# Optimization experiments

Hardware: AMD Instinct MI355X
Metric: run time of the kernel (lower is better)

## Reference

```python
import jax, jax.numpy as jnp
import numpy as np

COS_EPS = 1e-08


def setup_inputs() -> dict:
    key = jax.random.key(0)
    k1, k2, k3, k4, k5 = jax.random.split(key, 5)
    B, N, C = 4, 4096, 128
    q_node = jax.random.normal(k1, (B, N, C), dtype=jnp.float32)
    k_node = jax.random.normal(k2, (B, N, C), dtype=jnp.float32)
    v_node = jax.random.normal(k3, (B, N, C), dtype=jnp.float32)
    # shared Linear(h_dim, h_dim): torch default init scale ~ 1/sqrt(C)
    W = jax.random.normal(k4, (C, C), dtype=jnp.float32) / jnp.sqrt(jnp.float32(C))
    b = jax.random.normal(k5, (C,), dtype=jnp.float32) / jnp.sqrt(jnp.float32(C))
    return {"q_node": q_node, "k_node": k_node, "v_node": v_node, "W": W, "b": b}


def reference(q_node, k_node, v_node, W, b):
    # shared projection applied to q, k, v
    q = jnp.einsum('bnc,cd->bnd', q_node, W.T) + b
    k = jnp.einsum('bnc,cd->bnd', k_node, W.T) + b
    v = jnp.einsum('bnc,cd->bnd', v_node, W.T) + b
    # cosine similarity scores: [B, Nq, Nk]
    qn = jnp.linalg.norm(q, axis=2, keepdims=True)        # [B, Nq, 1]
    kn = jnp.linalg.norm(k, axis=2, keepdims=True)        # [B, Nk, 1]
    scores = jnp.einsum('bqc,bkc->bqk', q, k)
    cos_sim = scores / (qn * jnp.swapaxes(kn, 1, 2) + COS_EPS)
    # sum-normalization (not softmax)
    edge_weight = cos_sim / (cos_sim.sum(axis=2, keepdims=True) + 1e-08)
    # weighted aggregation: [B, Nq, C]
    return jnp.einsum('bqk,bkc->bqc', edge_weight, v)
```

## Files before the change

kernel.cpp:

```cpp
#include <hip/hip_runtime.h>

#define BB 4
#define NN 4096
#define CC 128
#define NROWS (BB * NN)

#define QN_OFF  0
#define QP_OFF  (QN_OFF + NROWS)
#define MM_OFF  (QP_OFF + NROWS * CC)
#define KS_OFF  (MM_OFF + BB * CC * CC)
#define PP_OFF  (KS_OFF + BB * CC)
#define KP_OFF  (PP_OFF + 256 * CC * CC)

__device__ __forceinline__ void fma4(float4& a, const float4 x,
    const float4 w0, const float4 w1, const float4 w2, const float4 w3)
{
    a.x += x.x * w0.x + x.y * w1.x + x.z * w2.x + x.w * w3.x;
    a.y += x.x * w0.y + x.y * w1.y + x.z * w2.y + x.w * w3.y;
    a.z += x.x * w0.z + x.y * w1.z + x.z * w2.z + x.w * w3.z;
    a.w += x.x * w0.w + x.y * w1.w + x.z * w2.w + x.w * w3.w;
}

__device__ __forceinline__ float dot4(const float4 x, const float4 k)
{
    return x.x * k.x + x.y * k.y + x.z * k.z + x.w * k.w;
}

__global__ __launch_bounds__(512, 2) void projpb_kernel(
    const float* __restrict__ q_node, const float* __restrict__ k_node,
    const float* __restrict__ v_node, const float* __restrict__ W,
    const float* __restrict__ bias, float* __restrict__ ws)
{
    __shared__ float S[CC * CC];
    __shared__ float4 red[512];
    const int tid = threadIdx.x;

    for (int e = tid; e < CC * CC; e += 512) {
        int d = e >> 7, c = e & 127;
        S[(c << 7) + ((((d >> 2) ^ (c & 31)) << 2) | (d & 3))] = W[e];
    }

    const int blk  = blockIdx.x;
    const int base = blk * 64;
    const int dg = tid & 31;
    const int rg = tid >> 5;

    float4 bias4 = ((const float4*)bias)[dg];
    float4 acc[8];
#pragma unroll
    for (int i = 0; i < 8; i++) acc[i] = bias4;

    __syncthreads();

    const float4* Qv = (const float4*)(q_node + (size_t)(base + rg * 4) * CC);
    const float4* Kv = (const float4*)(k_node + (size_t)(base + rg * 4) * CC);
    const float4* Sv = (const float4*)S;

#define LW(s0, s1, s2, s3, c)                              \
    s0 = Sv[(((c) + 0) << 5) + (dg ^ (((c) + 0) & 31))];   \
    s1 = Sv[(((c) + 1) << 5) + (dg ^ (((c) + 1) & 31))];   \
    s2 = Sv[(((c) + 2) << 5) + (dg ^ (((c) + 2) & 31))];   \
    s3 = Sv[(((c) + 3) << 5) + (dg ^ (((c) + 3) & 31))];
#define LX(xq, xk, c)                                      \
    { const int c4_ = (c) >> 2;                            \
      xq[0] = Qv[c4_];      xq[1] = Qv[32 + c4_];          \
      xq[2] = Qv[64 + c4_]; xq[3] = Qv[96 + c4_];          \
      xk[0] = Kv[c4_];      xk[1] = Kv[32 + c4_];          \
      xk[2] = Kv[64 + c4_]; xk[3] = Kv[96 + c4_]; }
#define FM(w0, w1, w2, w3, xq, xk)                         \
    fma4(acc[0], xq[0], w0, w1, w2, w3);                   \
    fma4(acc[1], xq[1], w0, w1, w2, w3);                   \
    fma4(acc[2], xq[2], w0, w1, w2, w3);                   \
    fma4(acc[3], xq[3], w0, w1, w2, w3);                   \
    fma4(acc[4], xk[0], w0, w1, w2, w3);                   \
    fma4(acc[5], xk[1], w0, w1, w2, w3);                   \
    fma4(acc[6], xk[2], w0, w1, w2, w3);                   \
    fma4(acc[7], xk[3], w0, w1, w2, w3);

    {
        float4 wA0, wA1, wA2, wA3, wB0, wB1, wB2, wB3;
        float4 xqA[4], xkA[4], xqB[4], xkB[4];

        LW(wA0, wA1, wA2, wA3, 0)
        LX(xqA, xkA, 0)
        for (int c = 0; c <= CC - 16; c += 8) {
            LW(wB0, wB1, wB2, wB3, c + 4)
            LX(xqB, xkB, c + 4)
            FM(wA0, wA1, wA2, wA3, xqA, xkA)
            LW(wA0, wA1, wA2, wA3, c + 8)
            LX(xqA, xkA, c + 8)
            FM(wB0, wB1, wB2, wB3, xqB, xkB)
        }
        LW(wB0, wB1, wB2, wB3, CC - 4)
        LX(xqB, xkB, CC - 4)
        FM(wA0, wA1, wA2, wA3, xqA, xkA)
        FM(wB0, wB1, wB2, wB3, xqB, xkB)
    }
#undef LW
#undef LX
#undef FM

#pragma unroll
    for (int i = 0; i < 4; i++) {
        const int rq = base + rg * 4 + i;
        float ss = acc[i].x * acc[i].x + acc[i].y * acc[i].y
                 + acc[i].z * acc[i].z + acc[i].w * acc[i].w;
#pragma unroll
        for (int off = 16; off > 0; off >>= 1) ss += __shfl_xor(ss, off, 32);
        ((float4*)(ws + QP_OFF + (size_t)rq * CC))[dg] = acc[i];
        if (dg == 0) ws[QN_OFF + rq] = sqrtf(ss);
    }

    __syncthreads();

    float* Khs = S;
    float* Vs  = S + 8192;

#pragma unroll
    for (int i = 0; i < 4; i++) {
        float ss = acc[4 + i].x * acc[4 + i].x + acc[4 + i].y * acc[4 + i].y
                 + acc[4 + i].z * acc[4 + i].z + acc[4 + i].w * acc[4 + i].w;
#pragma unroll
        for (int off = 16; off > 0; off >>= 1) ss += __shfl_xor(ss, off, 32);
        float inv = 1.0f / sqrtf(ss);
        float4 o = acc[4 + i];
        o.x *= inv; o.y *= inv; o.z *= inv; o.w *= inv;
        ((float4*)(Khs + (rg * 4 + i) * CC))[dg] = o;
    }

    const int c4v = tid & 31, nrv = tid >> 5;
    const float* Vp = v_node + (size_t)base * CC;
#pragma unroll
    for (int i = 0; i < 4; i++) {
        int n = nrv + i * 16;
        ((float4*)(Vs + n * CC))[c4v] = ((const float4*)(Vp + (size_t)n * CC))[c4v];
    }
    __syncthreads();

    float4 ksum4 = make_float4(0.f, 0.f, 0.f, 0.f);
#pragma unroll
    for (int i = 0; i < 4; i++) {
        int n = nrv + i * 16;
        float4 kv = ((const float4*)(Khs + n * CC))[c4v];
        ksum4.x += kv.x; ksum4.y += kv.y; ksum4.z += kv.z; ksum4.w += kv.w;
    }

    const int dg2 = tid & 15, cg = tid >> 4;
    float a2[4][8];
#pragma unroll
    for (int i = 0; i < 4; i++)
#pragma unroll
        for (int j = 0; j < 8; j++) a2[i][j] = 0.f;

#define P2L(ka, va, vb, n)                                  \
    ka = *(const float4*)(Khs + (n) * CC + 4 * cg);         \
    va = *(const float4*)(Vs + (n) * CC + 4 * dg2);         \
    vb = *(const float4*)(Vs + (n) * CC + 64 + 4 * dg2);
#define P2F(ka, va, vb)                                     \
    {  float kc[4] = {ka.x, ka.y, ka.z, ka.w};              \
       float vd[8] = {va.x, va.y, va.z, va.w,               \
                      vb.x, vb.y, vb.z, vb.w};              \
       _Pragma("unroll")                                    \
       for (int i = 0; i < 4; i++)                          \
           { _Pragma("unroll")                              \
             for (int j = 0; j < 8; j++)                    \
                 a2[i][j] += kc[i] * vd[j]; } }

    {
        float4 kaA, vaA, vbA, kaB, vaB, vbB;
        P2L(kaA, vaA, vbA, 0)
        for (int n = 0; n <= 60; n += 2) {
            P2L(kaB, vaB, vbB, n + 1)
            P2F(kaA, vaA, vbA)
            P2L(kaA, vaA, vbA, n + 2)
            P2F(kaB, vaB, vbB)
        }
        P2L(kaB, vaB, vbB, 63)
        P2F(kaA, vaA, vbA)
        P2F(kaB, vaB, vbB)
    }
#undef P2L
#undef P2F

    float* pp = ws + PP_OFF + (size_t)blk * (CC * CC);
#pragma unroll
    for (int i = 0; i < 4; i++) {
        int c = 4 * cg + i;
        *(float4*)(pp + c * CC + 4 * dg2) =
            make_float4(a2[i][0], a2[i][1], a2[i][2], a2[i][3]);
        *(float4*)(pp + c * CC + 64 + 4 * dg2) =
            make_float4(a2[i][4], a2[i][5], a2[i][6], a2[i][7]);
    }

    red[nrv * 32 + c4v] = ksum4;
    __syncthreads();
    if (tid < 32) {
        float4 sm = red[tid];
#pragma unroll
        for (int i = 1; i < 16; i++) {
            float4 t = red[i * 32 + tid];
            sm.x += t.x; sm.y += t.y; sm.z += t.z; sm.w += t.w;
        }
        ((float4*)(ws + KP_OFF + (size_t)blk * CC))[tid] = sm;
    }
}

__global__ __launch_bounds__(256) void mchain_kernel(const float* __restrict__ W,
                                                     const float* __restrict__ bias,
                                                     float* __restrict__ ws)
{
    __shared__ float4 W4s[CC * 32];
    __shared__ float m0row[2][CC];
    __shared__ float kpart[4];
    __shared__ float ksl[2];
    const int tid = threadIdx.x;
    const int b = blockIdx.y, x = blockIdx.x;
    const int c0 = x * 2;

    for (int idx = tid; idx < CC * 32; idx += 256) {
        int e = idx >> 5, d4 = idx & 31;
        W4s[(e << 5) + (d4 ^ (e & 31))] = ((const float4*)W)[idx];
    }

    {
        const int r = tid >> 7, d = tid & 127;
        const float* pp = ws + PP_OFF + (size_t)(b * 64) * (CC * CC)
                        + (size_t)(c0 + r) * CC + d;
        float a0 = 0.f, a1 = 0.f, a2 = 0.f, a3 = 0.f;
#pragma unroll 8
        for (int p = 0; p < 64; p += 4) {
            a0 += pp[(size_t)(p + 0) * (CC * CC)];
            a1 += pp[(size_t)(p + 1) * (CC * CC)];
            a2 += pp[(size_t)(p + 2) * (CC * CC)];
            a3 += pp[(size_t)(p + 3) * (CC * CC)];
        }
        m0row[r][d] = (a0 + a1) + (a2 + a3);
    }

    {
        const int rr = tid >> 7, p = tid & 127;
        float v = 0.f;
        if (p < 64) v = ws[KP_OFF + (size_t)(b * 64 + p) * CC + c0 + rr];
#pragma unroll
        for (int off = 32; off > 0; off >>= 1) v += __shfl_xor(v, off, 64);
        if ((tid & 63) == 0) kpart[tid >> 6] = v;
    }
    __syncthreads();
    if (tid < 2) {
        float s = kpart[tid * 2] + kpart[tid * 2 + 1];
        ksl[tid] = s;
        ws[KS_OFF + b * CC + c0 + tid] = s;
    }
    __syncthreads();

    const int r = tid >> 7, e = tid & 127;
    const float4* mr = (const float4*)m0row[r];
    float m = 0.f;
#pragma unroll
    for (int d4 = 0; d4 < 32; d4++) {
        float4 a4 = mr[d4];
        float4 w4 = W4s[(e << 5) + (d4 ^ (e & 31))];
        m += a4.x * w4.x + a4.y * w4.y + a4.z * w4.z + a4.w * w4.w;
    }
    m += ksl[r] * bias[e];
    ws[MM_OFF + (size_t)b * CC * CC + (size_t)(c0 + r) * CC + e] = m;
}

__global__ __launch_bounds__(512, 2) void out_kernel(const float* __restrict__ ws,
                                                     float* __restrict__ out)
{
    __shared__ float Ml[CC * CC];

    const int blk = blockIdx.x;
    const int b = blk >> 6;
    const int r0 = (blk & 63) * 64;
    const float* M = ws + MM_OFF + (size_t)b * CC * CC;
    const int tid = threadIdx.x;

    for (int e = tid; e < CC * CC / 4; e += 512)
        ((float4*)Ml)[e] = ((const float4*)M)[e];

    const float4* Ks4 = (const float4*)(ws + KS_OFF + b * CC);
    const int dg = tid & 31, rg = tid >> 5;
    const int row = r0 + rg * 4;
    const float4* Qv = (const float4*)(ws + QP_OFF + ((size_t)b * NN + row) * CC);
    const float4* Mv = (const float4*)Ml;

    float4 acc[4];
    float s[4];
#pragma unroll
    for (int i = 0; i < 4; i++) {
        acc[i] = make_float4(0.f, 0.f, 0.f, 0.f);
        s[i] = 0.f;
    }

    __syncthreads();

#define OLW(m0, m1, m2, m3, ks, c)               \
    m0 = Mv[(((c) + 0) << 5) + dg];              \
    m1 = Mv[(((c) + 1) << 5) + dg];              \
    m2 = Mv[(((c) + 2) << 5) + dg];              \
    m3 = Mv[(((c) + 3) << 5) + dg];              \
    ks = Ks4[(c) >> 2];
#define OLX(xv, c)                                 \
    { const int c4_ = (c) >> 2;                    \
      xv[0] = Qv[c4_];      xv[1] = Qv[32 + c4_];  \
      xv[2] = Qv[64 + c4_]; xv[3] = Qv[96 + c4_]; }
#define OFM(m0, m1, m2, m3, ks, xv)                  \
    _Pragma("unroll")                                \
    for (int i_ = 0; i_ < 4; i_++) {                 \
        fma4(acc[i_], xv[i_], m0, m1, m2, m3);       \
        s[i_] += dot4(xv[i_], ks);                   \
    }

    {
        float4 mA0, mA1, mA2, mA3, mB0, mB1, mB2, mB3;
        float4 ksA, ksB, xA[4], xB[4];
        OLW(mA0, mA1, mA2, mA3, ksA, 0)
        OLX(xA, 0)
        for (int c = 0; c <= CC - 16; c += 8) {
            OLW(mB0, mB1, mB2, mB3, ksB, c + 4)
            OLX(xB, c + 4)
            OFM(mA0, mA1, mA2, mA3, ksA, xA)
            OLW(mA0, mA1, mA2, mA3, ksA, c + 8)
            OLX(xA, c + 8)
            OFM(mB0, mB1, mB2, mB3, ksB, xB)
        }
        OLW(mB0, mB1, mB2, mB3, ksB, CC - 4)
        OLX(xB, CC - 4)
        OFM(mA0, mA1, mA2, mA3, ksA, xA)
        OFM(mB0, mB1, mB2, mB3, ksB, xB)
    }
#undef OLW
#undef OLX
#undef OFM

    float* op = out + ((size_t)b * NN + row) * CC;
    const float* qn = ws + QN_OFF + (size_t)b * NN + row;
#pragma unroll
    for (int i = 0; i < 4; i++) {
        float inv = 1.0f / (s[i] + 1e-8f * qn[i]);
        float4 o = acc[i];
        o.x *= inv; o.y *= inv; o.z *= inv; o.w *= inv;
        ((float4*)(op + (size_t)i * CC))[dg] = o;
    }
}

extern "C" void kernel_launch(void* const* d_in, const int* in_sizes, int n_in,
                              void* d_out, int out_size, void* d_ws, size_t ws_size,
                              hipStream_t stream)
{
    const float* q_node = (const float*)d_in[0];
    const float* k_node = (const float*)d_in[1];
    const float* v_node = (const float*)d_in[2];
    const float* W      = (const float*)d_in[3];
    const float* bias   = (const float*)d_in[4];
    float* out = (float*)d_out;
    float* ws  = (float*)d_ws;

    projpb_kernel<<<256, 512, 0, stream>>>(q_node, k_node, v_node, W, bias, ws);
    mchain_kernel<<<dim3(64, BB), 256, 0, stream>>>(W, bias, ws);
    out_kernel<<<256, 512, 0, stream>>>(ws, out);
}
```

Measured before the change: 130.6 us.

## Fuse three kernels into one persistent kernel with software grid barriers

Merges the projection/partial-product, M-chain, and output kernels into a single 256-block launch separated by atomic-counter grid barriers, with a memset resetting the counters each call. The M-chain stage is remapped onto 512-thread blocks by splitting the 64-way partial sum into two halves. The aim is to remove two kernel launch gaps and their tail effects. In exchange it relies on all 256 blocks being co-resident, which holds on a 256-CU part, and adds a memset plus spin-wait cost.

```diff
diff --git a/kernel.cpp b/kernel.cpp
--- a/kernel.cpp
+++ b/kernel.cpp
@@ -11,6 +11,9 @@
 #define KS_OFF  (MM_OFF + BB * CC * CC)
 #define PP_OFF  (KS_OFF + BB * CC)
 #define KP_OFF  (PP_OFF + 256 * CC * CC)
+#define BAR_OFF (KP_OFF + 256 * CC)
+
+#define NBLK 256
 
 __device__ __forceinline__ void fma4(float4& a, const float4 x,
     const float4 w0, const float4 w1, const float4 w2, const float4 w3)
@@ -26,35 +29,51 @@
     return x.x * k.x + x.y * k.y + x.z * k.z + x.w * k.w;
 }
 
-__global__ __launch_bounds__(512, 2) void projpb_kernel(
+__device__ __forceinline__ void grid_barrier(unsigned* ctr)
+{
+    __syncthreads();
+    __threadfence();
+    if (threadIdx.x == 0) {
+        atomicAdd(ctr, 1u);
+        while (atomicAdd(ctr, 0u) < NBLK) {}
+    }
+    __syncthreads();
+    __threadfence();
+}
+
+__global__ __launch_bounds__(512, 2) void fused_kernel(
     const float* __restrict__ q_node, const float* __restrict__ k_node,
     const float* __restrict__ v_node, const float* __restrict__ W,
-    const float* __restrict__ bias, float* __restrict__ ws)
+    const float* __restrict__ bias, float* __restrict__ ws,
+    float* __restrict__ out)
 {
     __shared__ float S[CC * CC];
     __shared__ float4 red[512];
+    unsigned* bar = (unsigned*)(ws + BAR_OFF);
+
     const int tid = threadIdx.x;
-
-    for (int e = tid; e < CC * CC; e += 512) {
-        int d = e >> 7, c = e & 127;
-        S[(c << 7) + ((((d >> 2) ^ (c & 31)) << 2) | (d & 3))] = W[e];
-    }
-
-    const int blk  = blockIdx.x;
-    const int base = blk * 64;
-    const int dg = tid & 31;
-    const int rg = tid >> 5;
-
-    float4 bias4 = ((const float4*)bias)[dg];
-    float4 acc[8];
-#pragma unroll
-    for (int i = 0; i < 8; i++) acc[i] = bias4;
-
-    __syncthreads();
-
-    const float4* Qv = (const float4*)(q_node + (size_t)(base + rg * 4) * CC);
-    const float4* Kv = (const float4*)(k_node + (size_t)(base + rg * 4) * CC);
-    const float4* Sv = (const float4*)S;
+    const int blk = blockIdx.x;
+
+    {
+        for (int e = tid; e < CC * CC; e += 512) {
+            int d = e >> 7, c = e & 127;
+            S[(c << 7) + ((((d >> 2) ^ (c & 31)) << 2) | (d & 3))] = W[e];
+        }
+
+        const int base = blk * 64;
+        const int dg = tid & 31;
+        const int rg = tid >> 5;
+
+        float4 bias4 = ((const float4*)bias)[dg];
+        float4 acc[8];
+#pragma unroll
+        for (int i = 0; i < 8; i++) acc[i] = bias4;
+
+        __syncthreads();
+
+        const float4* Qv = (const float4*)(q_node + (size_t)(base + rg * 4) * CC);
+        const float4* Kv = (const float4*)(k_node + (size_t)(base + rg * 4) * CC);
+        const float4* Sv = (const float4*)S;
 
 #define LW(s0, s1, s2, s3, c)                              \
     s0 = Sv[(((c) + 0) << 5) + (dg ^ (((c) + 0) & 31))];   \
@@ -77,83 +96,83 @@
     fma4(acc[6], xk[2], w0, w1, w2, w3);                   \
     fma4(acc[7], xk[3], w0, w1, w2, w3);
 
-    {
-        float4 wA0, wA1, wA2, wA3, wB0, wB1, wB2, wB3;
-        float4 xqA[4], xkA[4], xqB[4], xkB[4];
-
-        LW(wA0, wA1, wA2, wA3, 0)
-        LX(xqA, xkA, 0)
-        for (int c = 0; c <= CC - 16; c += 8) {
-            LW(wB0, wB1, wB2, wB3, c + 4)
-            LX(xqB, xkB, c + 4)
+        {
+            float4 wA0, wA1, wA2, wA3, wB0, wB1, wB2, wB3;
+            float4 xqA[4], xkA[4], xqB[4], xkB[4];
+
+            LW(wA0, wA1, wA2, wA3, 0)
+            LX(xqA, xkA, 0)
+            for (int c = 0; c <= CC - 16; c += 8) {
+                LW(wB0, wB1, wB2, wB3, c + 4)
+                LX(xqB, xkB, c + 4)
+                FM(wA0, wA1, wA2, wA3, xqA, xkA)
+                LW(wA0, wA1, wA2, wA3, c + 8)
+                LX(xqA, xkA, c + 8)
+                FM(wB0, wB1, wB2, wB3, xqB, xkB)
+            }
+            LW(wB0, wB1, wB2, wB3, CC - 4)
+            LX(xqB, xkB, CC - 4)
             FM(wA0, wA1, wA2, wA3, xqA, xkA)
-            LW(wA0, wA1, wA2, wA3, c + 8)
-            LX(xqA, xkA, c + 8)
             FM(wB0, wB1, wB2, wB3, xqB, xkB)
         }
-        LW(wB0, wB1, wB2, wB3, CC - 4)
-        LX(xqB, xkB, CC - 4)
-        FM(wA0, wA1, wA2, wA3, xqA, xkA)
-        FM(wB0, wB1, wB2, wB3, xqB, xkB)
-    }
 #undef LW
 #undef LX
 #undef FM
 
 #pragma unroll
-    for (int i = 0; i < 4; i++) {
-        const int rq = base + rg * 4 + i;
-        float ss = acc[i].x * acc[i].x + acc[i].y * acc[i].y
-                 + acc[i].z * acc[i].z + acc[i].w * acc[i].w;
-#pragma unroll
-        for (int off = 16; off > 0; off >>= 1) ss += __shfl_xor(ss, off, 32);
-        ((float4*)(ws + QP_OFF + (size_t)rq * CC))[dg] = acc[i];
-        if (dg == 0) ws[QN_OFF + rq] = sqrtf(ss);
-    }
-
-    __syncthreads();
-
-    float* Khs = S;
-    float* Vs  = S + 8192;
-
-#pragma unroll
-    for (int i = 0; i < 4; i++) {
-        float ss = acc[4 + i].x * acc[4 + i].x + acc[4 + i].y * acc[4 + i].y
-                 + acc[4 + i].z * acc[4 + i].z + acc[4 + i].w * acc[4 + i].w;
-#pragma unroll
-        for (int off = 16; off > 0; off >>= 1) ss += __shfl_xor(ss, off, 32);
-        float inv = 1.0f / sqrtf(ss);
-        float4 o = acc[4 + i];
-        o.x *= inv; o.y *= inv; o.z *= inv; o.w *= inv;
-        ((float4*)(Khs + (rg * 4 + i) * CC))[dg] = o;
-    }
-
-    const int c4v = tid & 31, nrv = tid >> 5;
-    const float* Vp = v_node + (size_t)base * CC;
-#pragma unroll
-    for (int i = 0; i < 4; i++) {
-        int n = nrv + i * 16;
-        ((float4*)(Vs + n * CC))[c4v] = ((const float4*)(Vp + (size_t)n * CC))[c4v];
-    }
-    __syncthreads();
-
-    float4 ksum4 = make_float4(0.f, 0.f, 0.f, 0.f);
-#pragma unroll
-    for (int i = 0; i < 4; i++) {
-        int n = nrv + i * 16;
-        float4 kv = ((const float4*)(Khs + n * CC))[c4v];
-        ksum4.x += kv.x; ksum4.y += kv.y; ksum4.z += kv.z; ksum4.w += kv.w;
-    }
-
-    const int dg2 = tid & 15, cg = tid >> 4;
-    float a2[4][8];
-#pragma unroll
-    for (int i = 0; i < 4; i++)
-#pragma unroll
-        for (int j = 0; j < 8; j++) a2[i][j] = 0.f;
+        for (int i = 0; i < 4; i++) {
+            const int rq = base + rg * 4 + i;
+            float ss = acc[i].x * acc[i].x + acc[i].y * acc[i].y
+                     + acc[i].z * acc[i].z + acc[i].w * acc[i].w;
+#pragma unroll
+            for (int off = 16; off > 0; off >>= 1) ss += __shfl_xor(ss, off, 32);
+            ((float4*)(ws + QP_OFF + (size_t)rq * CC))[dg] = acc[i];
+            if (dg == 0) ws[QN_OFF + rq] = sqrtf(ss);
+        }
+
+        __syncthreads();
+
+        float* Khs = S;
+        float* Vs  = S + 8192;
+
+#pragma unroll
+        for (int i = 0; i < 4; i++) {
+            float ss = acc[4 + i].x * acc[4 + i].x + acc[4 + i].y * acc[4 + i].y
+                     + acc[4 + i].z * acc[4 + i].z + acc[4 + i].w * acc[4 + i].w;
+#pragma unroll
+            for (int off = 16; off > 0; off >>= 1) ss += __shfl_xor(ss, off, 32);
+            float inv = 1.0f / sqrtf(ss);
+            float4 o = acc[4 + i];
+            o.x *= inv; o.y *= inv; o.z *= inv; o.w *= inv;
+            ((float4*)(Khs + (rg * 4 + i) * CC))[dg] = o;
+        }
+
+        const int c4v = tid & 31, nrv = tid >> 5;
+        const float* Vp = v_node + (size_t)base * CC;
+#pragma unroll
+        for (int i = 0; i < 4; i++) {
+            int n = nrv + i * 16;
+            ((float4*)(Vs + n * CC))[c4v] = ((const float4*)(Vp + (size_t)n * CC))[c4v];
+        }
+        __syncthreads();
+
+        float4 ksum4 = make_float4(0.f, 0.f, 0.f, 0.f);
+#pragma unroll
+        for (int i = 0; i < 4; i++) {
+            int n = nrv + i * 16;
+            float4 kv = ((const float4*)(Khs + n * CC))[c4v];
+            ksum4.x += kv.x; ksum4.y += kv.y; ksum4.z += kv.z; ksum4.w += kv.w;
+        }
+
+        const int dg2 = tid & 15, cg2 = tid >> 4;
+        float a2[4][8];
+#pragma unroll
+        for (int i = 0; i < 4; i++)
+#pragma unroll
+            for (int j = 0; j < 8; j++) a2[i][j] = 0.f;
 
 #define P2L(ka, va, vb, n)                                  \
-    ka = *(const float4*)(Khs + (n) * CC + 4 * cg);         \
+    ka = *(const float4*)(Khs + (n) * CC + 4 * cg2);        \
     va = *(const float4*)(Vs + (n) * CC + 4 * dg2);         \
     vb = *(const float4*)(Vs + (n) * CC + 64 + 4 * dg2);
 #define P2F(ka, va, vb)                                     \
@@ -166,135 +185,139 @@
              for (int j = 0; j < 8; j++)                    \
                  a2[i][j] += kc[i] * vd[j]; } }
 
-    {
-        float4 kaA, vaA, vbA, kaB, vaB, vbB;
-        P2L(kaA, vaA, vbA, 0)
-        for (int n = 0; n <= 60; n += 2) {
-            P2L(kaB, vaB, vbB, n + 1)
+        {
+            float4 kaA, vaA, vbA, kaB, vaB, vbB;
+            P2L(kaA, vaA, vbA, 0)
+            for (int n = 0; n <= 60; n += 2) {
+                P2L(kaB, vaB, vbB, n + 1)
+                P2F(kaA, vaA, vbA)
+                P2L(kaA, vaA, vbA, n + 2)
+                P2F(kaB, vaB, vbB)
+            }
+            P2L(kaB, vaB, vbB, 63)
             P2F(kaA, vaA, vbA)
-            P2L(kaA, vaA, vbA, n + 2)
             P2F(kaB, vaB, vbB)
         }
-        P2L(kaB, vaB, vbB, 63)
-        P2F(kaA, vaA, vbA)
-        P2F(kaB, vaB, vbB)
-    }
 #undef P2L
 #undef P2F
 
-    float* pp = ws + PP_OFF + (size_t)blk * (CC * CC);
-#pragma unroll
-    for (int i = 0; i < 4; i++) {
-        int c = 4 * cg + i;
-        *(float4*)(pp + c * CC + 4 * dg2) =
-            make_float4(a2[i][0], a2[i][1], a2[i][2], a2[i][3]);
-        *(float4*)(pp + c * CC + 64 + 4 * dg2) =
-            make_float4(a2[i][4], a2[i][5], a2[i][6], a2[i][7]);
-    }
-
-    red[nrv * 32 + c4v] = ksum4;
-    __syncthreads();
-    if (tid < 32) {
-        float4 sm = red[tid];
-#pragma unroll
-        for (int i = 1; i < 16; i++) {
-            float4 t = red[i * 32 + tid];
-            sm.x += t.x; sm.y += t.y; sm.z += t.z; sm.w += t.w;
-        }
-        ((float4*)(ws + KP_OFF + (size_t)blk * CC))[tid] = sm;
-    }
-}
-
-__global__ __launch_bounds__(256) void mchain_kernel(const float* __restrict__ W,
-                                                     const float* __restrict__ bias,
-                                                     float* __restrict__ ws)
-{
-    __shared__ float4 W4s[CC * 32];
-    __shared__ float m0row[2][CC];
-    __shared__ float kpart[4];
-    __shared__ float ksl[2];
-    const int tid = threadIdx.x;
-    const int b = blockIdx.y, x = blockIdx.x;
-    const int c0 = x * 2;
-
-    for (int idx = tid; idx < CC * 32; idx += 256) {
-        int e = idx >> 5, d4 = idx & 31;
-        W4s[(e << 5) + (d4 ^ (e & 31))] = ((const float4*)W)[idx];
-    }
+        float* pp = ws + PP_OFF + (size_t)blk * (CC * CC);
+#pragma unroll
+        for (int i = 0; i < 4; i++) {
+            int c = 4 * cg2 + i;
+            *(float4*)(pp + c * CC + 4 * dg2) =
+                make_float4(a2[i][0], a2[i][1], a2[i][2], a2[i][3]);
+            *(float4*)(pp + c * CC + 64 + 4 * dg2) =
+                make_float4(a2[i][4], a2[i][5], a2[i][6], a2[i][7]);
+        }
+
+        red[nrv * 32 + c4v] = ksum4;
+        __syncthreads();
+        if (tid < 32) {
+            float4 sm = red[tid];
+#pragma unroll
+            for (int i = 1; i < 16; i++) {
+                float4 t = red[i * 32 + tid];
+                sm.x += t.x; sm.y += t.y; sm.z += t.z; sm.w += t.w;
+            }
+            ((float4*)(ws + KP_OFF + (size_t)blk * CC))[tid] = sm;
+        }
+    }
+
+    grid_barrier(bar);
 
     {
-        const int r = tid >> 7, d = tid & 127;
-        const float* pp = ws + PP_OFF + (size_t)(b * 64) * (CC * CC)
-                        + (size_t)(c0 + r) * CC + d;
-        float a0 = 0.f, a1 = 0.f, a2 = 0.f, a3 = 0.f;
+        float4* W4s   = (float4*)S;
+        float*  m0p   = (float*)red;
+        float*  kpart = m0p + 512;
+        float*  ksl   = kpart + 2;
+        float*  m0row = ksl + 2;
+
+        const int x = blk & 63, b2 = blk >> 6;
+        const int c0 = x * 2;
+
+        for (int idx = tid; idx < CC * 32; idx += 512) {
+            int e = idx >> 5, d4 = idx & 31;
+            W4s[(e << 5) + (d4 ^ (e & 31))] = ((const float4*)W)[idx];
+        }
+
+        {
+            const int r2 = tid >> 7;
+            const int r = r2 & 1, h = r2 >> 1;
+            const int d = tid & 127;
+            const float* pp = ws + PP_OFF
+                            + (size_t)(b2 * 64 + h * 32) * (CC * CC)
+                            + (size_t)(c0 + r) * CC + d;
+            float a0 = 0.f, a1 = 0.f, a2 = 0.f, a3 = 0.f;
 #pragma unroll 8
-        for (int p = 0; p < 64; p += 4) {
-            a0 += pp[(size_t)(p + 0) * (CC * CC)];
-            a1 += pp[(size_t)(p + 1) * (CC * CC)];
-            a2 += pp[(size_t)(p + 2) * (CC * CC)];
-            a3 += pp[(size_t)(p + 3) * (CC * CC)];
-        }
-        m0row[r][d] = (a0 + a1) + (a2 + a3);
-    }
+            for (int p = 0; p < 32; p += 4) {
+                a0 += pp[(size_t)(p + 0) * (CC * CC)];
+                a1 += pp[(size_t)(p + 1) * (CC * CC)];
+                a2 += pp[(size_t)(p + 2) * (CC * CC)];
+                a3 += pp[(size_t)(p + 3) * (CC * CC)];
+            }
+            m0p[r2 * CC + d] = (a0 + a1) + (a2 + a3);
+        }
+
+        if (tid < 128) {
+            const int rr = tid >> 6, p = tid & 63;
+            float v = ws[KP_OFF + (size_t)(b2 * 64 + p) * CC + c0 + rr];
+#pragma unroll
+            for (int off = 32; off > 0; off >>= 1) v += __shfl_xor(v, off, 64);
+            if ((tid & 63) == 0) kpart[rr] = v;
+        }
+        __syncthreads();
+
+        if (tid < 256) {
+            const int r = tid >> 7, d = tid & 127;
+            m0row[r * CC + d] = m0p[r * CC + d] + m0p[(r + 2) * CC + d];
+        }
+        if (tid < 2) {
+            ksl[tid] = kpart[tid];
+            ws[KS_OFF + b2 * CC + c0 + tid] = kpart[tid];
+        }
+        __syncthreads();
+
+        if (tid < 256) {
+            const int r = tid >> 7, e = tid & 127;
+            const float4* mr = (const float4*)(m0row + r * CC);
+            float m = 0.f;
+#pragma unroll
+            for (int d4 = 0; d4 < 32; d4++) {
+                float4 a4 = mr[d4];
+                float4 w4 = W4s[(e << 5) + (d4 ^ (e & 31))];
+                m += a4.x * w4.x + a4.y * w4.y + a4.z * w4.z + a4.w * w4.w;
+            }
+            m += ksl[r] * bias[e];
+            ws[MM_OFF + (size_t)b2 * CC * CC + (size_t)(c0 + r) * CC + e] = m;
+        }
+    }
+
+    grid_barrier(bar + 1);
 
     {
-        const int rr = tid >> 7, p = tid & 127;
-        float v = 0.f;
-        if (p < 64) v = ws[KP_OFF + (size_t)(b * 64 + p) * CC + c0 + rr];
-#pragma unroll
-        for (int off = 32; off > 0; off >>= 1) v += __shfl_xor(v, off, 64);
-        if ((tid & 63) == 0) kpart[tid >> 6] = v;
-    }
-    __syncthreads();
-    if (tid < 2) {
-        float s = kpart[tid * 2] + kpart[tid * 2 + 1];
-        ksl[tid] = s;
-        ws[KS_OFF + b * CC + c0 + tid] = s;
-    }
-    __syncthreads();
-
-    const int r = tid >> 7, e = tid & 127;
-    const float4* mr = (const float4*)m0row[r];
-    float m = 0.f;
-#pragma unroll
-    for (int d4 = 0; d4 < 32; d4++) {
-        float4 a4 = mr[d4];
-        float4 w4 = W4s[(e << 5) + (d4 ^ (e & 31))];
-        m += a4.x * w4.x + a4.y * w4.y + a4.z * w4.z + a4.w * w4.w;
-    }
-    m += ksl[r] * bias[e];
-    ws[MM_OFF + (size_t)b * CC * CC + (size_t)(c0 + r) * CC + e] = m;
-}
-
-__global__ __launch_bounds__(512, 2) void out_kernel(const float* __restrict__ ws,
-                                                     float* __restrict__ out)
-{
-    __shared__ float Ml[CC * CC];
-
-    const int blk = blockIdx.x;
-    const int b = blk >> 6;
-    const int r0 = (blk & 63) * 64;
-    const float* M = ws + MM_OFF + (size_t)b * CC * CC;
-    const int tid = threadIdx.x;
-
-    for (int e = tid; e < CC * CC / 4; e += 512)
-        ((float4*)Ml)[e] = ((const float4*)M)[e];
-
-    const float4* Ks4 = (const float4*)(ws + KS_OFF + b * CC);
-    const int dg = tid & 31, rg = tid >> 5;
-    const int row = r0 + rg * 4;
-    const float4* Qv = (const float4*)(ws + QP_OFF + ((size_t)b * NN + row) * CC);
-    const float4* Mv = (const float4*)Ml;
-
-    float4 acc[4];
-    float s[4];
-#pragma unroll
-    for (int i = 0; i < 4; i++) {
-        acc[i] = make_float4(0.f, 0.f, 0.f, 0.f);
-        s[i] = 0.f;
-    }
-
-    __syncthreads();
+        const int b = blk >> 6;
+        const int r0 = (blk & 63) * 64;
+        const float* M = ws + MM_OFF + (size_t)b * CC * CC;
+
+        for (int e = tid; e < CC * CC / 4; e += 512)
+            ((float4*)S)[e] = ((const float4*)M)[e];
+
+        const float4* Ks4 = (const float4*)(ws + KS_OFF + b * CC);
+        const int dg = tid & 31, rg = tid >> 5;
+        const int row = r0 + rg * 4;
+        const float4* Qv = (const float4*)(ws + QP_OFF + ((size_t)b * NN + row) * CC);
+        const float4* Mv = (const float4*)S;
+
+        float4 acc[4];
+        float s[4];
+#pragma unroll
+        for (int i = 0; i < 4; i++) {
+            acc[i] = make_float4(0.f, 0.f, 0.f, 0.f);
+            s[i] = 0.f;
+        }
+
+        __syncthreads();
 
 #define OLW(m0, m1, m2, m3, ks, c)               \
     m0 = Mv[(((c) + 0) << 5) + dg];              \
@@ -313,36 +336,37 @@
         s[i_] += dot4(xv[i_], ks);                   \
     }
 
-    {
-        float4 mA0, mA1, mA2, mA3, mB0, mB1, mB2, mB3;
-        float4 ksA, ksB, xA[4], xB[4];
-        OLW(mA0, mA1, mA2, mA3, ksA, 0)
-        OLX(xA, 0)
-        for (int c = 0; c <= CC - 16; c += 8) {
-            OLW(mB0, mB1, mB2, mB3, ksB, c + 4)
-            OLX(xB, c + 4)
+        {
+            float4 mA0, mA1, mA2, mA3, mB0, mB1, mB2, mB3;
+            float4 ksA, ksB, xA[4], xB[4];
+            OLW(mA0, mA1, mA2, mA3, ksA, 0)
+            OLX(xA, 0)
+            for (int c = 0; c <= CC - 16; c += 8) {
+                OLW(mB0, mB1, mB2, mB3, ksB, c + 4)
+                OLX(xB, c + 4)
+                OFM(mA0, mA1, mA2, mA3, ksA, xA)
+                OLW(mA0, mA1, mA2, mA3, ksA, c + 8)
+                OLX(xA, c + 8)
+                OFM(mB0, mB1, mB2, mB3, ksB, xB)
+            }
+            OLW(mB0, mB1, mB2, mB3, ksB, CC - 4)
+            OLX(xB, CC - 4)
             OFM(mA0, mA1, mA2, mA3, ksA, xA)
-            OLW(mA0, mA1, mA2, mA3, ksA, c + 8)
-            OLX(xA, c + 8)
             OFM(mB0, mB1, mB2, mB3, ksB, xB)
         }
-        OLW(mB0, mB1, mB2, mB3, ksB, CC - 4)
-        OLX(xB, CC - 4)
-        OFM(mA0, mA1, mA2, mA3, ksA, xA)
-        OFM(mB0, mB1, mB2, mB3, ksB, xB)
-    }
 #undef OLW
 #undef OLX
 #undef OFM
 
-    float* op = out + ((size_t)b * NN + row) * CC;
-    const float* qn = ws + QN_OFF + (size_t)b * NN + row;
-#pragma unroll
-    for (int i = 0; i < 4; i++) {
-        float inv = 1.0f / (s[i] + 1e-8f * qn[i]);
-        float4 o = acc[i];
-        o.x *= inv; o.y *= inv; o.z *= inv; o.w *= inv;
-        ((float4*)(op + (size_t)i * CC))[dg] = o;
+        float* op = out + ((size_t)b * NN + row) * CC;
+        const float* qn = ws + QN_OFF + (size_t)b * NN + row;
+#pragma unroll
+        for (int i = 0; i < 4; i++) {
+            float inv = 1.0f / (s[i] + 1e-8f * qn[i]);
+            float4 o = acc[i];
+            o.x *= inv; o.y *= inv; o.z *= inv; o.w *= inv;
+            ((float4*)(op + (size_t)i * CC))[dg] = o;
+        }
     }
 }
 
@@ -358,7 +382,8 @@
     float* out = (float*)d_out;
     float* ws  = (float*)d_ws;
 
-    projpb_kernel<<<256, 512, 0, stream>>>(q_node, k_node, v_node, W, bias, ws);
-    mchain_kernel<<<dim3(64, BB), 256, 0, stream>>>(W, bias, ws);
-    out_kernel<<<256, 512, 0, stream>>>(ws, out);
-}
+    hipMemsetAsync(ws + BAR_OFF, 0, 2 * sizeof(unsigned), stream);
+
+    fused_kernel<<<NBLK, 512, 0, stream>>>(q_node, k_node, v_node,
+                                           W, bias, ws, out);
+}
```

After: 272.3 us. +108.5%, slower.
